# Kernel optimization log

Hardware: AMD Instinct MI355X
Metric: run time of the kernel (lower is better)

Reference implementation:

```python
import jax, jax.numpy as jnp
import numpy as np
from jax import lax

CAM_EDGE = 4096


def setup_inputs() -> dict:
    key = jax.random.key(0)
    x1 = jax.random.normal(key, (CAM_EDGE, CAM_EDGE), dtype=jnp.float32)
    return {"x1": x1}


def _label_components(mask):
    """4-connected component labeling via iterative min-label propagation.

    mask: [E, E] bool. Returns int32 [E, E] labels: each masked cell gets the
    minimum linear index of its connected component; unmasked cells get the
    sentinel N = E*E.
    """
    E = mask.shape[0]
    N = E * E
    sent = jnp.int32(N)
    init = jnp.where(mask, jnp.arange(N, dtype=jnp.int32).reshape(E, E), sent)
    sent_row = jnp.full((1, E), sent, dtype=jnp.int32)
    sent_col = jnp.full((E, 1), sent, dtype=jnp.int32)

    def propagate(lab):
        dn = jnp.concatenate([sent_row, lab[:-1]], axis=0)   # neighbor from above
        up = jnp.concatenate([lab[1:], sent_row], axis=0)    # neighbor from below
        lf = jnp.concatenate([sent_col, lab[:, :-1]], axis=1)
        rt = jnp.concatenate([lab[:, 1:], sent_col], axis=1)
        m = jnp.minimum(jnp.minimum(lab, up), jnp.minimum(dn, jnp.minimum(lf, rt)))
        return jnp.where(mask, m, sent)

    def cond(carry):
        _, changed = carry
        return changed

    def body(carry):
        lab, _ = carry
        new = propagate(lab)
        return new, jnp.any(new != lab)

    labels, _ = lax.while_loop(cond, body, (init, jnp.array(True)))
    return labels


def reference(x1):
    E = x1.shape[0]
    N = E * E
    v = jnp.tanh(x1)
    mask = v > 0
    labels = _label_components(mask)          # [E, E] int32, sentinel N for masked-out
    flat_lab = labels.reshape(-1)
    vflat = jnp.where(mask, v, 0.0).reshape(-1)
    ones = mask.reshape(-1).astype(v.dtype)
    # bucket N+1 collects the sentinel (non-positive cells); drop it
    sums = jax.ops.segment_sum(vflat, flat_lab, num_segments=N + 1)[:N]
    counts = jax.ops.segment_sum(ones, flat_lab, num_segments=N + 1)[:N]
    has = counts > 0                          # one True per connected component (its root index)
    per_comp = jnp.where(has, sums / (N + 1 - counts), 0.0)
    n_comp = jnp.sum(has.astype(v.dtype))
    total = jnp.sum(per_comp)
    return jnp.where(n_comp > 0, total / n_comp, 0.0)
```

## Files before the change

### kernel.cpp

```cpp
#include <hip/hip_runtime.h>

#define EDGE 4096
#define NPIX (EDGE * EDGE)
#define TILES_X 64
#define NTILES (TILES_X * TILES_X)
#define SLOTS 2048

static __device__ __forceinline__ int g_load(int* L, int i) {
    return __hip_atomic_load(&L[i], __ATOMIC_RELAXED, __HIP_MEMORY_SCOPE_AGENT);
}
static __device__ __forceinline__ int g_find(int* L, int i) {
    int p = g_load(L, i);
    while (p != i) { i = p; p = g_load(L, i); }
    return i;
}
static __device__ int g_unite(int* L, int a, int b) {
    while (true) {
        a = g_find(L, a); b = g_find(L, b);
        if (a == b) return 0;
        const int lo = a < b ? a : b;
        const int hi = a ^ b ^ lo;
        const int old = atomicMin(&L[hi], lo);
        if (old == hi) return 1;
        a = lo; b = old;
    }
}

static __device__ __forceinline__ int l_load(int* L, int i) {
    return __hip_atomic_load(&L[i], __ATOMIC_RELAXED, __HIP_MEMORY_SCOPE_WORKGROUP);
}
static __device__ __forceinline__ int l_find(int* L, int i) {
    int p = l_load(L, i);
    while (p != i) { i = p; p = l_load(L, i); }
    return i;
}
static __device__ void l_unite(int* L, int a, int b) {
    while (true) {
        a = l_find(L, a); b = l_find(L, b);
        if (a == b) return;
        const int lo = a < b ? a : b;
        const int hi = a ^ b ^ lo;
        const int old = atomicMin(&L[hi], lo);
        if (old == hi) return;
        a = lo; b = old;
    }
}
static __device__ __forceinline__ int l_find_plain(const int* L, int i) {
    int p = L[i];
    while (p != i) { i = p; p = L[i]; }
    return i;
}

__global__ __launch_bounds__(256) void k_tile(const float* __restrict__ x,
                                              int* __restrict__ G,
                                              int* __restrict__ topM, int* __restrict__ botM,
                                              int* __restrict__ leftM, int* __restrict__ rightM,
                                              int* __restrict__ rootsArr,
                                              double* __restrict__ partials) {
    __shared__ unsigned long long mrow[64];
    __shared__ unsigned int mpart[64][4];
    __shared__ int lab[4096];
    __shared__ int wtot[4];
    __shared__ double wsum[4];
    const int t = threadIdx.x;
    const int tile = blockIdx.x;
    const int tr = tile >> 6, tc = tile & 63;

    const int r = t >> 2, qd = t & 3;
    const float4* xp = reinterpret_cast<const float4*>(
        x + ((size_t)((tr << 6) | r) << 12) + (tc << 6) + (qd << 4));
    unsigned int m16 = 0;
    float sf = 0.0f;
    #pragma unroll
    for (int k = 0; k < 4; ++k) {
        const float4 a = xp[k];
        const float vv[4] = {a.x, a.y, a.z, a.w};
        #pragma unroll
        for (int j = 0; j < 4; ++j) {
            const float v = vv[j];
            if (v > 0.0f) {
                m16 |= 1u << (k * 4 + j);
                const float e = __expf(2.0f * v);
                sf += 1.0f - 2.0f / (e + 1.0f);
            }
        }
    }
    mpart[r][qd] = m16;
    double s = (double)sf;
    for (int off = 32; off > 0; off >>= 1) s += __shfl_down(s, off, 64);
    if ((t & 63) == 0) wsum[t >> 6] = s;
    __syncthreads();
    if (t < 64) {
        mrow[t] = (unsigned long long)mpart[t][0]
                | ((unsigned long long)mpart[t][1] << 16)
                | ((unsigned long long)mpart[t][2] << 32)
                | ((unsigned long long)mpart[t][3] << 48);
    }
    if (t == 0) partials[tile] = wsum[0] + wsum[1] + wsum[2] + wsum[3];
    __syncthreads();

    #pragma unroll
    for (int q = 0; q < 16; ++q) {
        const int lp = t + (q << 8);
        const int rr = lp >> 6, j = lp & 63;
        const unsigned long long m = mrow[rr];
        int v = 0x7FFFFFFF;
        if ((m >> j) & 1ull) {
            const unsigned long long sb = ~m & ((1ull << j) - 1ull);
            const int start = sb ? (64 - __builtin_clzll(sb)) : 0;
            v = (rr << 6) | start;
        }
        lab[lp] = v;
    }
    __syncthreads();

    {
        const int rr = t >> 2;
        if (rr >= 1) {
            const unsigned long long m = mrow[rr], u = mrow[rr - 1];
            unsigned long long vm = m & u & ~((m << 1) & (u << 1));
            const int cb = (t & 3) * 16;
            vm = (vm >> cb) & 0xFFFFull;
            while (vm) {
                const int j = __builtin_ctzll(vm) + cb;
                l_unite(lab, (rr << 6) | j, ((rr - 1) << 6) | j);
                vm &= vm - 1;
            }
        }
    }
    __syncthreads();

    int broot = -1;
    {
        int rr, j;
        if (t < 64)       { rr = 0;       j = t; }
        else if (t < 128) { rr = 63;      j = t - 64; }
        else if (t < 192) { rr = t - 128; j = 0; }
        else              { rr = t - 192; j = 63; }
        if ((mrow[rr] >> j) & 1ull) broot = l_find_plain(lab, (rr << 6) | j);
    }
    int c = 0; unsigned int rmask = 0;
    #pragma unroll
    for (int q = 0; q < 16; ++q) {
        const int lp = t + (q << 8);
        if (lab[lp] == lp) { rmask |= 1u << q; ++c; }
    }

    int inc = c;
    #pragma unroll
    for (int off = 1; off < 64; off <<= 1) {
        const int v = __shfl_up(inc, off, 64);
        if ((t & 63) >= off) inc += v;
    }
    if ((t & 63) == 63) wtot[t >> 6] = inc;
    __syncthreads();
    const int w = t >> 6;
    int wbase = 0;
    if (w > 0) wbase += wtot[0];
    if (w > 1) wbase += wtot[1];
    if (w > 2) wbase += wtot[2];
    const int my_base = wbase + inc - c;
    const int nroots = wtot[0] + wtot[1] + wtot[2] + wtot[3];

    const int tileBase = tile * SLOTS;
    {
        int k = 0;
        #pragma unroll
        for (int q = 0; q < 16; ++q) {
            if ((rmask >> q) & 1u) {
                lab[t + (q << 8)] = my_base + k; ++k;
            }
        }
    }
    for (int i = t; i < nroots; i += 256) G[tileBase + i] = tileBase + i;
    __syncthreads();

    {
        const int node = (broot >= 0) ? (tileBase + lab[broot]) : -1;
        const int idx = (tile << 6) | (t & 63);
        if (t < 64)       topM[idx]   = node;
        else if (t < 128) botM[idx]   = node;
        else if (t < 192) leftM[idx]  = node;
        else              rightM[idx] = node;
    }
    if (t == 0) rootsArr[tile] = nroots;
}

__global__ __launch_bounds__(128) void k_xmerge(const int* __restrict__ topM,
                                                const int* __restrict__ botM,
                                                const int* __restrict__ leftM,
                                                const int* __restrict__ rightM,
                                                int* G, int* __restrict__ linksArr) {
    __shared__ int lsum[2];
    const int t = threadIdx.x, tile = blockIdx.x;
    const int tr = tile >> 6, tc = tile & 63;
    int links = 0;
    if (t < 64) {
        if (tr > 0) {
            const int a = topM[(tile << 6) | t];
            const int b = botM[((tile - 64) << 6) | t];
            if ((a | b) >= 0) {
                bool redund = false;
                if (t > 0) {
                    const int ap = topM[(tile << 6) | (t - 1)];
                    const int bp = botM[((tile - 64) << 6) | (t - 1)];
                    redund = ((ap & bp) >= 0) ? false : false;
                    redund = (ap >= 0) && (bp >= 0);
                }
                if (!redund) links = g_unite(G, a, b);
            }
        }
    } else {
        const int rr = t - 64;
        if (tc > 0) {
            const int a = leftM[(tile << 6) | rr];
            const int b = rightM[((tile - 1) << 6) | rr];
            if ((a | b) >= 0) {
                bool redund = false;
                if (rr > 0) {
                    const int ap = leftM[(tile << 6) | (rr - 1)];
                    const int bp = rightM[((tile - 1) << 6) | (rr - 1)];
                    redund = (ap >= 0) && (bp >= 0);
                }
                if (!redund) links = g_unite(G, a, b);
            }
        }
    }
    for (int off = 32; off > 0; off >>= 1) links += __shfl_down(links, off, 64);
    if ((t & 63) == 0) lsum[t >> 6] = links;
    __syncthreads();
    if (t == 0) linksArr[tile] = lsum[0] + lsum[1];
}

__global__ __launch_bounds__(256) void k_final(const double* __restrict__ partials,
                                               const int* __restrict__ rootsArr,
                                               const int* __restrict__ linksArr,
                                               float* __restrict__ out) {
    __shared__ double sd[256];
    __shared__ int si[256];
    const int t = threadIdx.x;
    double s = 0.0; int n = 0;
    for (int i = t; i < NTILES; i += 256) {
        s += partials[i];
        n += rootsArr[i] - linksArr[i];
    }
    sd[t] = s; si[t] = n; __syncthreads();
    for (int off = 128; off > 0; off >>= 1) {
        if (t < off) { sd[t] += sd[t + off]; si[t] += si[t + off]; }
        __syncthreads();
    }
    if (t == 0) {
        const int nn = si[0];
        out[0] = (nn > 0) ? (float)(sd[0] / (double)(NPIX + 1) / (double)nn) : 0.0f;
    }
}

extern "C" void kernel_launch(void* const* d_in, const int* in_sizes, int n_in,
                              void* d_out, int out_size, void* d_ws, size_t ws_size,
                              hipStream_t stream) {
    const float* x = (const float*)d_in[0];
    float* out = (float*)d_out;

    char* ws = (char*)d_ws;
    int* G = (int*)ws;
    int* topM   = (int*)(ws + (32u << 20));
    int* botM   = topM  + NTILES * 64;
    int* leftM  = botM  + NTILES * 64;
    int* rightM = leftM + NTILES * 64;
    double* partials = (double*)(ws + (36u << 20));
    int* rootsArr = (int*)(ws + (36u << 20) + (64u << 10));
    int* linksArr = (int*)(ws + (36u << 20) + (80u << 10));

    k_tile  <<<NTILES, 256, 0, stream>>>(x, G, topM, botM, leftM, rightM,
                                         rootsArr, partials);
    k_xmerge<<<NTILES, 128, 0, stream>>>(topM, botM, leftM, rightM, G, linksArr);
    k_final <<<1, 256, 0, stream>>>(partials, rootsArr, linksArr, out);
}
```

Before: 61.57 us.

## Label horizontal runs instead of pixels in tile-local union-find

The per-tile union-find now runs over horizontal runs of set pixels instead of over all 4096 pixels. Run starts come from bit tricks, rows are given a prefix-sum base, and vertical unions use popcount to map a column to its run index. This removes the 4096-entry label init and the full-pixel root scan, shrinking shared memory use and work. The cross-tile merge also reads the previous neighbor through wave shuffles instead of reloading it from global memory. Border nodes now need popcount lookups, and the root scans loop over a variable run count.

```diff
diff --git a/kernel.cpp b/kernel.cpp
--- a/kernel.cpp
+++ b/kernel.cpp
@@ -58,10 +58,13 @@
                                               int* __restrict__ rootsArr,
                                               double* __restrict__ partials) {
     __shared__ unsigned long long mrow[64];
+    __shared__ unsigned long long rstart[64];
     __shared__ unsigned int mpart[64][4];
-    __shared__ int lab[4096];
+    __shared__ int rowbase[64];
+    __shared__ int P[SLOTS];
     __shared__ int wtot[4];
     __shared__ double wsum[4];
+    __shared__ int Rtot;
     const int t = threadIdx.x;
     const int tile = blockIdx.x;
     const int tr = tile >> 6, tc = tile & 63;
@@ -90,41 +93,54 @@
     for (int off = 32; off > 0; off >>= 1) s += __shfl_down(s, off, 64);
     if ((t & 63) == 0) wsum[t >> 6] = s;
     __syncthreads();
+
     if (t < 64) {
-        mrow[t] = (unsigned long long)mpart[t][0]
-                | ((unsigned long long)mpart[t][1] << 16)
-                | ((unsigned long long)mpart[t][2] << 32)
-                | ((unsigned long long)mpart[t][3] << 48);
+        const unsigned long long m =
+              (unsigned long long)mpart[t][0]
+            | ((unsigned long long)mpart[t][1] << 16)
+            | ((unsigned long long)mpart[t][2] << 32)
+            | ((unsigned long long)mpart[t][3] << 48);
+        mrow[t] = m;
+        const unsigned long long rs = m & ~(m << 1);
+        rstart[t] = rs;
+        int inc = __popcll(rs);
+        const int nr = inc;
+        #pragma unroll
+        for (int off = 1; off < 64; off <<= 1) {
+            const int v = __shfl_up(inc, off, 64);
+            if (t >= off) inc += v;
+        }
+        rowbase[t] = inc - nr;
+        if (t == 63) Rtot = inc;
     }
     if (t == 0) partials[tile] = wsum[0] + wsum[1] + wsum[2] + wsum[3];
     __syncthreads();
 
-    #pragma unroll
-    for (int q = 0; q < 16; ++q) {
-        const int lp = t + (q << 8);
-        const int rr = lp >> 6, j = lp & 63;
-        const unsigned long long m = mrow[rr];
-        int v = 0x7FFFFFFF;
-        if ((m >> j) & 1ull) {
-            const unsigned long long sb = ~m & ((1ull << j) - 1ull);
-            const int start = sb ? (64 - __builtin_clzll(sb)) : 0;
-            v = (rr << 6) | start;
-        }
-        lab[lp] = v;
-    }
+    const int R = Rtot;
+    for (int i = t; i < R; i += 256) P[i] = i;
     __syncthreads();
 
     {
         const int rr = t >> 2;
         if (rr >= 1) {
             const unsigned long long m = mrow[rr], u = mrow[rr - 1];
-            unsigned long long vm = m & u & ~((m << 1) & (u << 1));
+            const unsigned long long vm = m & u;
+            unsigned long long st = vm & ~(vm << 1);
             const int cb = (t & 3) * 16;
-            vm = (vm >> cb) & 0xFFFFull;
-            while (vm) {
-                const int j = __builtin_ctzll(vm) + cb;
-                l_unite(lab, (rr << 6) | j, ((rr - 1) << 6) | j);
-                vm &= vm - 1;
+            st = (st >> cb) & 0xFFFFull;
+            if (st) {
+                const unsigned long long rs  = rstart[rr];
+                const unsigned long long rsu = rstart[rr - 1];
+                const int rb  = rowbase[rr];
+                const int rbu = rowbase[rr - 1];
+                do {
+                    const int j = __builtin_ctzll(st) + cb;
+                    const unsigned long long thru = ~0ull >> (63 - j);
+                    const int na = rb  + __popcll(rs  & thru) - 1;
+                    const int nb = rbu + __popcll(rsu & thru) - 1;
+                    l_unite(P, na, nb);
+                    st &= st - 1;
+                } while (st);
             }
         }
     }
@@ -137,46 +153,41 @@
         else if (t < 128) { rr = 63;      j = t - 64; }
         else if (t < 192) { rr = t - 128; j = 0; }
         else              { rr = t - 192; j = 63; }
-        if ((mrow[rr] >> j) & 1ull) broot = l_find_plain(lab, (rr << 6) | j);
-    }
-    int c = 0; unsigned int rmask = 0;
-    #pragma unroll
-    for (int q = 0; q < 16; ++q) {
-        const int lp = t + (q << 8);
-        if (lab[lp] == lp) { rmask |= 1u << q; ++c; }
-    }
-
-    int inc = c;
+        if ((mrow[rr] >> j) & 1ull) {
+            const int idx = __popcll(rstart[rr] & (~0ull >> (63 - j))) - 1;
+            broot = l_find_plain(P, rowbase[rr] + idx);
+        }
+    }
+    __syncthreads();
+
+    int c = 0;
+    for (int i = t; i < R; i += 256) c += (P[i] == i);
+    int inc2 = c;
     #pragma unroll
     for (int off = 1; off < 64; off <<= 1) {
-        const int v = __shfl_up(inc, off, 64);
-        if ((t & 63) >= off) inc += v;
-    }
-    if ((t & 63) == 63) wtot[t >> 6] = inc;
+        const int v = __shfl_up(inc2, off, 64);
+        if ((t & 63) >= off) inc2 += v;
+    }
+    if ((t & 63) == 63) wtot[t >> 6] = inc2;
     __syncthreads();
     const int w = t >> 6;
     int wbase = 0;
     if (w > 0) wbase += wtot[0];
     if (w > 1) wbase += wtot[1];
     if (w > 2) wbase += wtot[2];
-    const int my_base = wbase + inc - c;
+    const int my_base = wbase + inc2 - c;
     const int nroots = wtot[0] + wtot[1] + wtot[2] + wtot[3];
 
     const int tileBase = tile * SLOTS;
     {
-        int k = 0;
-        #pragma unroll
-        for (int q = 0; q < 16; ++q) {
-            if ((rmask >> q) & 1u) {
-                lab[t + (q << 8)] = my_base + k; ++k;
-            }
-        }
+        int k = my_base;
+        for (int i = t; i < R; i += 256) if (P[i] == i) P[i] = k++;
     }
     for (int i = t; i < nroots; i += 256) G[tileBase + i] = tileBase + i;
     __syncthreads();
 
     {
-        const int node = (broot >= 0) ? (tileBase + lab[broot]) : -1;
+        const int node = (broot >= 0) ? (tileBase + P[broot]) : -1;
         const int idx = (tile << 6) | (t & 63);
         if (t < 64)       topM[idx]   = node;
         else if (t < 128) botM[idx]   = node;
@@ -199,14 +210,10 @@
         if (tr > 0) {
             const int a = topM[(tile << 6) | t];
             const int b = botM[((tile - 64) << 6) | t];
+            const int ap = __shfl_up(a, 1, 64);
+            const int bp = __shfl_up(b, 1, 64);
             if ((a | b) >= 0) {
-                bool redund = false;
-                if (t > 0) {
-                    const int ap = topM[(tile << 6) | (t - 1)];
-                    const int bp = botM[((tile - 64) << 6) | (t - 1)];
-                    redund = ((ap & bp) >= 0) ? false : false;
-                    redund = (ap >= 0) && (bp >= 0);
-                }
+                const bool redund = (t > 0) && ((ap | bp) >= 0);
                 if (!redund) links = g_unite(G, a, b);
             }
         }
@@ -215,13 +222,10 @@
         if (tc > 0) {
             const int a = leftM[(tile << 6) | rr];
             const int b = rightM[((tile - 1) << 6) | rr];
+            const int ap = __shfl_up(a, 1, 64);
+            const int bp = __shfl_up(b, 1, 64);
             if ((a | b) >= 0) {
-                bool redund = false;
-                if (rr > 0) {
-                    const int ap = leftM[(tile << 6) | (rr - 1)];
-                    const int bp = rightM[((tile - 1) << 6) | (rr - 1)];
-                    redund = (ap >= 0) && (bp >= 0);
-                }
+                const bool redund = (rr > 0) && ((ap | bp) >= 0);
                 if (!redund) links = g_unite(G, a, b);
             }
         }
```

Result: faster. 56.98 us (-7.5%).
